# Performance work log

Hardware: AMD Instinct MI355X
Metric: run time of the kernel (lower is better)

Reference implementation:

```python
import jax, jax.numpy as jnp
from jax import lax
import numpy as np

D_MODEL = 128
N_HEADS = 8
N_POINTS = 8
MAX_MAG = 10.0
NEG_SLOPE = 0.1


def conv2d(x, w, b, pad):
    # x: (N, Cin, H, W), w: (Cout, Cin, kh, kw)
    y = lax.conv_general_dilated(x, w, (1, 1), [(pad, pad), (pad, pad)],
                                 dimension_numbers=('NCHW', 'OIHW', 'NCHW'))
    return y + b[None, :, None, None]


def leaky(x):
    return jnp.where(x >= 0, x, NEG_SLOPE * x)


def bilinear_sample(img, grid):
    # img: (B, C, H, W); grid: (B, P, H, W, 2) in [-1, 1] (x, y)
    # Matches torch F.grid_sample(mode='bilinear', padding_mode='zeros', align_corners=False)
    B, C, H, W = img.shape
    x = ((grid[..., 0] + 1.0) * W - 1.0) * 0.5
    y = ((grid[..., 1] + 1.0) * H - 1.0) * 0.5
    x0 = jnp.floor(x)
    y0 = jnp.floor(y)
    wx1 = x - x0
    wy1 = y - y0

    def one(img_b, x0b, y0b, wx1b, wy1b):
        def gather(xi, yi):
            valid = (xi >= 0) & (xi < W) & (yi >= 0) & (yi < H)
            xc = jnp.clip(xi, 0, W - 1).astype(jnp.int32)
            yc = jnp.clip(yi, 0, H - 1).astype(jnp.int32)
            v = img_b[:, yc, xc]  # (C, P, H, W)
            return v * valid
        wx0b = 1.0 - wx1b
        wy0b = 1.0 - wy1b
        v00 = gather(x0b, y0b)
        v01 = gather(x0b + 1, y0b)
        v10 = gather(x0b, y0b + 1)
        v11 = gather(x0b + 1, y0b + 1)
        return (v00 * (wx0b * wy0b) + v01 * (wx1b * wy0b)
                + v10 * (wx0b * wy1b) + v11 * (wx1b * wy1b))

    return jax.vmap(one)(img, x0, y0, wx1, wy1)  # (B, C, P, H, W)


def ss_deform_attn(value, loc):
    # value: (N, nh, d, H, W); loc: (N, nh, P, H, W, 2) in normalized [0,1] coords
    N, nh, d, H, W = value.shape
    P = loc.shape[2]
    v = value.reshape(N * nh, d, H, W)
    grids = (2.0 * loc - 1.0).reshape(N * nh, P, H, W, 2)
    sampled = bilinear_sample(v, grids)  # (N*nh, d, P, H, W)
    # per-location attention logits = <sampled_point, value_at_location>
    scores = jnp.einsum('ndphw,ndhw->nphw', sampled, v)
    aw = jax.nn.softmax(scores, axis=1)
    out = jnp.einsum('ndphw,nphw->ndhw', sampled, aw)
    return out.reshape(N, nh * d, H, W)


def _forward(query, value, reference_points, co_w1, co_b1, co_w2, co_b2,
             co_w3, co_b3, co_w4, co_b4, val_w, val_b, out_w, out_b):
    N, C, H, W = value.shape
    v = conv2d(value, val_w, val_b, 0)
    v = v.reshape(N, N_HEADS, D_MODEL // N_HEADS, H, W)
    o = leaky(conv2d(query, co_w1, co_b1, 1))
    o = leaky(conv2d(o, co_w2, co_b2, 1))
    o = leaky(conv2d(o, co_w3, co_b3, 1))
    o = conv2d(o, co_w4, co_b4, 1)
    o = MAX_MAG * jnp.tanh(o)
    offsets = o.reshape(N, N_HEADS, N_POINTS, H, W, 2)
    norm = jnp.array([W, H], dtype=o.dtype)  # (x, y) normalizer
    loc = reference_points[:, None, None, :, :, :] + offsets / norm
    out = ss_deform_attn(v, loc)
    return conv2d(out, out_w, out_b, 0)


def setup_inputs() -> dict:
    key = jax.random.key(0)
    ks = jax.random.split(key, 12)
    N, H, W = 4, 80, 80

    def w_init(k, shape):
        fan_in = shape[1] * shape[2] * shape[3]
        return jax.random.normal(k, shape, jnp.float32) / np.sqrt(fan_in)

    return {
        'query': jax.random.normal(ks[0], (N, 2 * D_MODEL, H, W), jnp.float32),
        'value': jax.random.normal(ks[1], (N, D_MODEL, H, W), jnp.float32),
        'reference_points': jax.random.uniform(ks[2], (N, H, W, 2), jnp.float32),
        'co_w1': w_init(ks[3], (D_MODEL, 2 * D_MODEL, 3, 3)),
        'co_b1': jnp.zeros((D_MODEL,), jnp.float32),
        'co_w2': w_init(ks[4], (D_MODEL, D_MODEL, 3, 3)),
        'co_b2': jnp.zeros((D_MODEL,), jnp.float32),
        'co_w3': w_init(ks[5], (D_MODEL, D_MODEL, 3, 3)),
        'co_b3': jnp.zeros((D_MODEL,), jnp.float32),
        'co_w4': w_init(ks[6], (N_HEADS * N_POINTS * 2, D_MODEL, 3, 3)),
        'co_b4': jnp.zeros((N_HEADS * N_POINTS * 2,), jnp.float32),
        'val_w': w_init(ks[7], (D_MODEL, D_MODEL, 1, 1)),
        'val_b': jnp.zeros((D_MODEL,), jnp.float32),
        'out_w': w_init(ks[8], (D_MODEL, D_MODEL, 1, 1)),
        'out_b': jnp.zeros((D_MODEL,), jnp.float32),
    }


def reference(query, value, reference_points, co_w1, co_b1, co_w2, co_b2,
              co_w3, co_b3, co_w4, co_b4, val_w, val_b, out_w, out_b):
    return _forward(query, value, reference_points, co_w1, co_b1, co_w2, co_b2,
                    co_w3, co_b3, co_w4, co_b4, val_w, val_b, out_w, out_b)
```

## Files before the change

kernel.cpp:

```cpp
#include <hip/hip_runtime.h>
#include <math.h>

#define Hh 80
#define Ww 80
#define HW 6400
#define PS 6724
#define NB 4

typedef _Float16 half8 __attribute__((ext_vector_type(8)));
typedef _Float16 half4v __attribute__((ext_vector_type(4)));
typedef float f32x16 __attribute__((ext_vector_type(16)));

__device__ __forceinline__ void gload16(const _Float16* g, _Float16* l) {
    __builtin_amdgcn_global_load_lds(
        (const __attribute__((address_space(1))) void*)g,
        (__attribute__((address_space(3))) void*)l, 16, 0, 0);
}

#define WAITVM(N) asm volatile("s_waitcnt vmcnt(" #N ")" ::: "memory")

__device__ __forceinline__ void barrier_mem() {
    asm volatile("" ::: "memory");
    __builtin_amdgcn_s_barrier();
    asm volatile("" ::: "memory");
}

__device__ inline void wblob_one(const float* src, _Float16* dst, int CI, int d) {
    int NC = CI / 32;
    int j = d & 7;
    int l = (d >> 3) & 63;
    int h = (d >> 9) & 1;
    int rest = d >> 10;
    int tap = rest % 9;
    rest /= 9;
    int c = rest % NC;
    int CT = rest / NC;
    int co = CT * 32 + (l & 31);
    int ci = c * 32 + h * 16 + (l >> 5) * 8 + j;
    dst[d] = (_Float16)src[((size_t)co * CI + ci) * 9 + tap];
}

__device__ inline void wblob1x1_one(const float* src, _Float16* dst, int d) {
    int j = d & 7;
    int l = (d >> 3) & 63;
    int c = (d >> 9) & 7;
    int CT = d >> 12;
    int co = CT * 32 + (l & 31);
    int ci = c * 16 + (l >> 5) * 8 + j;
    dst[d] = (_Float16)src[co * 128 + ci];
}

__device__ inline int padsite(int p) {
    if (p < 82) return p;
    if (p < 164) return 81 * 82 + (p - 82);
    if (p < 244) return (p - 163) * 82;
    return (p - 243) * 82 + 81;
}

__global__ __launch_bounds__(256) void prep_all(
    const float* __restrict__ w1, const float* __restrict__ w2,
    const float* __restrict__ w3, const float* __restrict__ w4,
    const float* __restrict__ vw, const float* __restrict__ ow,
    _Float16* __restrict__ b1, _Float16* __restrict__ b2,
    _Float16* __restrict__ b3, _Float16* __restrict__ b4,
    _Float16* __restrict__ bv, _Float16* __restrict__ bo,
    int* __restrict__ qh_i, int* __restrict__ hA_i, int* __restrict__ hB_i,
    const float* __restrict__ query, const float* __restrict__ value,
    _Float16* __restrict__ q_h, _Float16* __restrict__ v_h) {
    __shared__ _Float16 T[64 * 264];
    const int blk = blockIdx.x;
    const int t = threadIdx.x;

    if (blk < 4304) {
        int idx = blk * 256 + t;
        if (idx < 294912) { wblob_one(w1, b1, 256, idx); return; }
        idx -= 294912;
        if (idx < 147456) { wblob_one(w2, b2, 128, idx); return; }
        idx -= 147456;
        if (idx < 147456) { wblob_one(w3, b3, 128, idx); return; }
        idx -= 147456;
        if (idx < 147456) { wblob_one(w4, b4, 128, idx); return; }
        idx -= 147456;
        if (idx < 16384) { wblob1x1_one(vw, bv, idx); return; }
        idx -= 16384;
        if (idx < 16384) { wblob1x1_one(ow, bo, idx); return; }
        idx -= 16384;
        if (idx < 165888) {
            int n = idx / 41472, rr = idx % 41472;
            int c = rr / 5184, r2 = rr % 5184;
            int p = r2 >> 4, k = r2 & 15;
            qh_i[((size_t)(n * 8 + c) * PS + padsite(p)) * 16 + k] = 0;
            return;
        }
        idx -= 165888;
        if (idx < 82944) {
            int n = idx / 20736, rr = idx % 20736;
            int c = rr / 5184, r2 = rr % 5184;
            int p = r2 >> 4, k = r2 & 15;
            hA_i[((size_t)(n * 4 + c) * PS + padsite(p)) * 16 + k] = 0;
            return;
        }
        idx -= 82944;
        if (idx < 82944) {
            int n = idx / 20736, rr = idx % 20736;
            int c = rr / 5184, r2 = rr % 5184;
            int p = r2 >> 4, k = r2 & 15;
            hB_i[((size_t)(n * 4 + c) * PS + padsite(p)) * 16 + k] = 0;
        }
        return;
    }

    if (blk < 4704) {
        const int b = blk - 4304;
        const int xcd = b & 7, n = xcd & 3, hi = xcd >> 2;
        const int s0 = hi * 3200 + (b >> 3) * 64;
        constexpr int CI = 256, ST = CI + 8;
        for (int idx = t; idx < 64 * CI; idx += 256) {
            int ci = idx >> 6, sl = idx & 63;
            T[sl * ST + ci] = (_Float16)query[((size_t)n * CI + ci) * HW + s0 + sl];
        }
        __syncthreads();
        for (int idx = t; idx < 64 * 32; idx += 256) {
            int q = idx & 31, sl = idx >> 5;
            int s = s0 + sl, yy = s / 80, xx = s % 80;
            int c = q >> 2, off = (q & 3) * 8;
            *(int4*)(q_h + ((size_t)(n * 8 + c) * PS + (yy + 1) * 82 + (xx + 1)) * 32 + off) =
                *(const int4*)(&T[sl * ST + q * 8]);
        }
        return;
    }

    {
        const int b = blk - 4704;
        const int xcd = b & 7, n = xcd & 3, hi = xcd >> 2;
        const int s0 = hi * 3200 + (b >> 3) * 64;
        constexpr int CI = 128, ST = CI + 8;
        for (int idx = t; idx < 64 * CI; idx += 256) {
            int ci = idx >> 6, sl = idx & 63;
            T[sl * ST + ci] = (_Float16)value[((size_t)n * CI + ci) * HW + s0 + sl];
        }
        __syncthreads();
        for (int idx = t; idx < 64 * 16; idx += 256) {
            int q = idx & 15, sl = idx >> 4;
            *(int4*)(v_h + ((size_t)n * HW + s0 + sl) * CI + q * 8) =
                *(const int4*)(&T[sl * ST + q * 8]);
        }
    }
}

template <int NCp, int ACT>
__global__ __launch_bounds__(256, 2) void conv3x3_mfma(
    const _Float16* __restrict__ in, const _Float16* __restrict__ wblob,
    const float* __restrict__ bias, void* __restrict__ outp) {
    constexpr int NS = NCp * 18;
    __shared__ _Float16 Abuf[2][24 * 512];
    __shared__ _Float16 Bbuf[2][6 * 1024];

    const int b = blockIdx.x;
    const int xcd = b & 7, n = xcd & 3, hi = xcd >> 2;
    const int r = b >> 3;
    const int x0 = (r % 5) * 16, y0 = hi * 40 + (r / 5) * 4;
    const int t = threadIdx.x;
    const int w = t >> 6, l = t & 63;
    const int lane31 = l & 31, lhalf = l >> 5;
    const int lx = lane31 & 15, lyw = lane31 >> 4;
    const int si = l & 15, g8 = l >> 4;

    const _Float16* bplane0 = in + (size_t)(n * NCp) * PS * 32;
    const _Float16* wA = wblob + (size_t)w * NS * 512 + l * 8;

    f32x16 acc0 = {}, acc1 = {};

    auto stageA = [&](int grp) {
        const _Float16* asrc = wA + (size_t)grp * 6 * 512;
        _Float16* adst = &Abuf[grp & 1][w * 512];
#pragma unroll
        for (int k2 = 0; k2 < 6; ++k2)
            gload16(asrc + (size_t)k2 * 512, adst + (size_t)(k2 * 4) * 512);
    };
    auto stageB = [&](const _Float16* plane, int par) {
#pragma unroll
        for (int j = 0; j < 3; ++j) {
            const int m = 3 * w + j, rr = m >> 1, sg = m & 1;
            gload16(plane + ((size_t)((y0 + rr) * 82 + x0 + sg * 16 + si)) * 32 + g8 * 8,
                    &Bbuf[par][rr * 1024 + sg * 512]);
        }
    };
    auto compute6 = [&](int gi, const _Float16* ab, const _Float16* bb) {
#pragma unroll
        for (int k = 0; k < 6; ++k) {
            const int u = gi * 6 + k;
            const int tap = u >> 1, h = u & 1;
            const int dy = tap / 3, dx = tap % 3;
            half8 a = *(const half8*)&ab[(k * 4 + w) * 512 + l * 8];
            const int cx = lx + dx;
            const int boff = (cx >> 4) * 512 + (h * 2 + lhalf) * 128 + (cx & 15) * 8;
            half8 b0 = *(const half8*)&bb[(lyw + dy) * 1024 + boff];
            half8 b1 = *(const half8*)&bb[(lyw + 2 + dy) * 1024 + boff];
            acc0 = __builtin_amdgcn_mfma_f32_32x32x16_f16(a, b0, acc0, 0, 0, 0);
            acc1 = __builtin_amdgcn_mfma_f32_32x32x16_f16(a, b1, acc1, 0, 0, 0);
        }
    };

    stageA(0);
    stageB(bplane0, 0);

    const _Float16* bplane = bplane0;
#pragma unroll 1
    for (int c = 0; c < NCp - 1; ++c) {
        const _Float16* bplaneN = bplane + (size_t)PS * 32;
        const _Float16* bb = Bbuf[c & 1];
        stageA(3 * c + 1);
        WAITVM(6);
        barrier_mem();
        compute6(0, Abuf[(3 * c) & 1], bb);
        barrier_mem();
        stageA(3 * c + 2);
        WAITVM(6);
        barrier_mem();
        compute6(1, Abuf[(3 * c + 1) & 1], bb);
        barrier_mem();
        stageA(3 * c + 3);
        stageB(bplaneN, (c + 1) & 1);
        WAITVM(9);
        barrier_mem();
        compute6(2, Abuf[(3 * c + 2) & 1], bb);
        barrier_mem();
        bplane = bplaneN;
    }
    {
        const int c = NCp - 1;
        const _Float16* bb = Bbuf[c & 1];
        stageA(3 * c + 1);
        WAITVM(6);
        barrier_mem();
        compute6(0, Abuf[(3 * c) & 1], bb);
        barrier_mem();
        stageA(3 * c + 2);
        WAITVM(6);
        barrier_mem();
        compute6(1, Abuf[(3 * c + 1) & 1], bb);
        barrier_mem();
        WAITVM(0);
        barrier_mem();
        compute6(2, Abuf[(3 * c + 2) & 1], bb);
    }

    const int x = x0 + lx;
#pragma unroll
    for (int f = 0; f < 2; ++f) {
        const f32x16& acc = f ? acc1 : acc0;
        const int y = y0 + lyw + 2 * f;
#pragma unroll
        for (int q = 0; q < 4; ++q) {
            const int inner = 8 * q + 4 * lhalf;
            const int co0 = w * 32 + inner;
            float v[4];
#pragma unroll
            for (int i = 0; i < 4; ++i) {
                float vv = acc[q * 4 + i] + bias[co0 + i];
                if (ACT == 1) vv = (vv >= 0.f) ? vv : 0.1f * vv;
                else vv = 10.f * tanhf(vv);
                v[i] = vv;
            }
            if (ACT == 1) {
                half4v hv = {(_Float16)v[0], (_Float16)v[1], (_Float16)v[2], (_Float16)v[3]};
                *(half4v*)((_Float16*)outp +
                    ((size_t)(n * 4 + w) * PS + (y + 1) * 82 + (x + 1)) * 32 + inner) = hv;
            } else {
                float4 fv = {v[0], v[1], v[2], v[3]};
                *(float4*)((float*)outp + ((size_t)n * HW + y * 80 + x) * 128 + co0) = fv;
            }
        }
    }
}

template <int MODE>
__global__ __launch_bounds__(256) void conv1x1_mfma(
    const _Float16* __restrict__ in, const _Float16* __restrict__ wblob,
    const float* __restrict__ bias, float* __restrict__ outp) {
    const int b = blockIdx.x;
    const int xcd = b & 7, n = xcd & 3, hi = xcd >> 2;
    const int r = b >> 3;
    const int coH = r & 1, strip = r >> 1;
    const int t = threadIdx.x;
    const int w = t >> 6, l = t & 63;
    const int lane31 = l & 31, lhalf = l >> 5;
    const int s = hi * 3200 + strip * 128 + w * 32 + lane31;

    const _Float16* pB = in + (size_t)(n * HW + s) * 128 + lhalf * 8;
    const _Float16* pA0 = wblob + (size_t)(coH * 2) * 8 * 512 + l * 8;
    const _Float16* pA1 = pA0 + 8 * 512;

    half8 bB[8], bA0[8], bA1[8];
#pragma unroll
    for (int c = 0; c < 8; ++c) {
        bB[c]  = *(const half8*)(pB + c * 16);
        bA0[c] = *(const half8*)(pA0 + (size_t)c * 512);
        bA1[c] = *(const half8*)(pA1 + (size_t)c * 512);
    }
    f32x16 acc0 = {}, acc1 = {};
#pragma unroll
    for (int c = 0; c < 8; ++c) {
        acc0 = __builtin_amdgcn_mfma_f32_32x32x16_f16(bA0[c], bB[c], acc0, 0, 0, 0);
        acc1 = __builtin_amdgcn_mfma_f32_32x32x16_f16(bA1[c], bB[c], acc1, 0, 0, 0);
    }

#pragma unroll
    for (int ct = 0; ct < 2; ++ct) {
        const f32x16& acc = ct ? acc1 : acc0;
#pragma unroll
        for (int q = 0; q < 4; ++q) {
            const int co0 = coH * 64 + ct * 32 + 8 * q + 4 * lhalf;
            if (MODE == 0) {
                const int hd = co0 >> 4, dd = co0 & 15;
                float4 fv = {acc[4 * q + 0] + bias[co0 + 0], acc[4 * q + 1] + bias[co0 + 1],
                             acc[4 * q + 2] + bias[co0 + 2], acc[4 * q + 3] + bias[co0 + 3]};
                *(float4*)&outp[((size_t)(n * 8 + hd) * HW + s) * 16 + dd] = fv;
            } else {
#pragma unroll
                for (int i = 0; i < 4; ++i)
                    outp[(size_t)(n * 128 + co0 + i) * HW + s] = acc[4 * q + i] + bias[co0 + i];
            }
        }
    }
}

__global__ __launch_bounds__(256, 2) void deform_attn_kernel(
    const float* __restrict__ v_s, const float* __restrict__ offs,
    const float* __restrict__ ref, _Float16* __restrict__ att) {
    const int slice = blockIdx.x;
    const int n = slice >> 3, hd = slice & 7;
    const int t = threadIdx.x;
    const int s = blockIdx.y * 64 + (t >> 2);
    const int d0 = (t & 3) * 4;
    const int nb = n * 8 + hd;
    const float* vbase = v_s + (size_t)nb * (HW * 16) + d0;

    const float4 cv = *(const float4*)&v_s[((size_t)nb * HW + s) * 16 + d0];
    const float rx = ref[(size_t)(n * HW + s) * 2 + 0] * 80.f - 0.5f;
    const float ry = ref[(size_t)(n * HW + s) * 2 + 1] * 80.f - 0.5f;

    const int e = (s >= 3200) ? 1 : 0;
    const float* ob0 = offs + ((size_t)n * HW + (2 * s - e * HW)) * 128 + hd * 16 + e;

    float4 oxv[4], oyv[4];
#pragma unroll
    for (int i = 0; i < 4; ++i) {
        oxv[i] = *(const float4*)(ob0 + i * 4);
        oyv[i] = *(const float4*)(ob0 + 128 + i * 4);
    }
    float ox[8], oy[8];
#pragma unroll
    for (int i = 0; i < 4; ++i) {
        ox[2 * i] = oxv[i].x; ox[2 * i + 1] = oxv[i].z;
        oy[2 * i] = oyv[i].x; oy[2 * i + 1] = oyv[i].z;
    }

    float wx1[8], wy1[8];
    int ix[8], iy[8];
#pragma unroll
    for (int p = 0; p < 8; ++p) {
        const float px = rx + ox[p];
        const float py = ry + oy[p];
        const float fx = floorf(px), fy = floorf(py);
        ix[p] = (int)fx; iy[p] = (int)fy;
        wx1[p] = px - fx; wy1[p] = py - fy;
    }

    float4 g[8][4];
#pragma unroll
    for (int p = 0; p < 8; ++p) {
        const int xc0 = min(max(ix[p], 0), 79),     xc1 = min(max(ix[p] + 1, 0), 79);
        const int yc0 = min(max(iy[p], 0), 79),     yc1 = min(max(iy[p] + 1, 0), 79);
        const int r0 = yc0 * 80, r1 = yc1 * 80;
        g[p][0] = *(const float4*)(vbase + (size_t)(r0 + xc0) * 16);
        g[p][1] = *(const float4*)(vbase + (size_t)(r0 + xc1) * 16);
        g[p][2] = *(const float4*)(vbase + (size_t)(r1 + xc0) * 16);
        g[p][3] = *(const float4*)(vbase + (size_t)(r1 + xc1) * 16);
    }

    float4 sampled[8];
    float score[8];
#pragma unroll
    for (int p = 0; p < 8; ++p) {
        const float vx0 = (ix[p] >= 0 && ix[p] < Ww) ? 1.f : 0.f;
        const float vx1 = (ix[p] + 1 >= 0 && ix[p] + 1 < Ww) ? 1.f : 0.f;
        const float vy0 = (iy[p] >= 0 && iy[p] < Hh) ? 1.f : 0.f;
        const float vy1 = (iy[p] + 1 >= 0 && iy[p] + 1 < Hh) ? 1.f : 0.f;
        const float wx0 = 1.f - wx1[p], wy0 = 1.f - wy1[p];
        const float w00 = wx0 * wy0 * vx0 * vy0;
        const float w01 = wx1[p] * wy0 * vx1 * vy0;
        const float w10 = wx0 * wy1[p] * vx0 * vy1;
        const float w11 = wx1[p] * wy1[p] * vx1 * vy1;
        float4 sv;
        sv.x = g[p][0].x * w00 + g[p][1].x * w01 + g[p][2].x * w10 + g[p][3].x * w11;
        sv.y = g[p][0].y * w00 + g[p][1].y * w01 + g[p][2].y * w10 + g[p][3].y * w11;
        sv.z = g[p][0].z * w00 + g[p][1].z * w01 + g[p][2].z * w10 + g[p][3].z * w11;
        sv.w = g[p][0].w * w00 + g[p][1].w * w01 + g[p][2].w * w10 + g[p][3].w * w11;
        sampled[p] = sv;
        float sc = sv.x * cv.x + sv.y * cv.y + sv.z * cv.z + sv.w * cv.w;
        sc += __shfl_xor(sc, 1);
        sc += __shfl_xor(sc, 2);
        score[p] = sc;
    }

    float m = score[0];
#pragma unroll
    for (int p = 1; p < 8; ++p) m = fmaxf(m, score[p]);
    float sum = 0.f, aw[8];
#pragma unroll
    for (int p = 0; p < 8; ++p) {
        aw[p] = __expf(score[p] - m);
        sum += aw[p];
    }
    const float inv = 1.f / sum;
    float4 o = {0.f, 0.f, 0.f, 0.f};
#pragma unroll
    for (int p = 0; p < 8; ++p) {
        o.x += aw[p] * sampled[p].x;
        o.y += aw[p] * sampled[p].y;
        o.z += aw[p] * sampled[p].z;
        o.w += aw[p] * sampled[p].w;
    }
    o.x *= inv; o.y *= inv; o.z *= inv; o.w *= inv;

    half4v hv = {(_Float16)o.x, (_Float16)o.y, (_Float16)o.z, (_Float16)o.w};
    *(half4v*)&att[((size_t)n * HW + s) * 128 + hd * 16 + d0] = hv;
}

extern "C" void kernel_launch(void* const* d_in, const int* in_sizes, int n_in,
                              void* d_out, int out_size, void* d_ws, size_t ws_size,
                              hipStream_t stream) {
    const float* query = (const float*)d_in[0];
    const float* value = (const float*)d_in[1];
    const float* ref   = (const float*)d_in[2];
    const float* co_w1 = (const float*)d_in[3];
    const float* co_b1 = (const float*)d_in[4];
    const float* co_w2 = (const float*)d_in[5];
    const float* co_b2 = (const float*)d_in[6];
    const float* co_w3 = (const float*)d_in[7];
    const float* co_b3 = (const float*)d_in[8];
    const float* co_w4 = (const float*)d_in[9];
    const float* co_b4 = (const float*)d_in[10];
    const float* val_w = (const float*)d_in[11];
    const float* val_b = (const float*)d_in[12];
    const float* out_w = (const float*)d_in[13];
    const float* out_b = (const float*)d_in[14];

    char* ws = (char*)d_ws;
    size_t o = 0;
    auto alloc = [&](size_t bytes) { char* p = ws + o; o += (bytes + 255) & ~(size_t)255; return p; };

    _Float16* wb2 = (_Float16*)alloc(147456 * 2);
    _Float16* wb3 = (_Float16*)alloc(147456 * 2);
    _Float16* wb4 = (_Float16*)alloc(147456 * 2);
    _Float16* wbv = (_Float16*)alloc(16384 * 2);
    _Float16* wbo = (_Float16*)alloc(16384 * 2);
    char* vsR = alloc(3276800 * 4);
    float* v_s = (float*)vsR;
    _Float16* wb1 = (_Float16*)vsR;
    _Float16* v_h = (_Float16*)alloc((size_t)NB * HW * 128 * 2);
    char* R1 = alloc((size_t)NB * 8 * PS * 32 * 2);
    _Float16* q_h = (_Float16*)R1;
    float* o4 = (float*)R1;
    char* R2 = alloc((size_t)NB * 4 * PS * 32 * 2 * 2);
    _Float16* hA = (_Float16*)R2;
    _Float16* hB = (_Float16*)(R2 + (size_t)NB * 4 * PS * 32 * 2);
    _Float16* att_h = (_Float16*)R2;

    prep_all<<<5104, 256, 0, stream>>>(co_w1, co_w2, co_w3, co_w4, val_w, out_w,
                                       wb1, wb2, wb3, wb4, wbv, wbo,
                                       (int*)q_h, (int*)hA, (int*)hB,
                                       query, value, q_h, v_h);

    conv3x3_mfma<8, 1><<<400, 256, 0, stream>>>(q_h, wb1, co_b1, hA);

    conv1x1_mfma<0><<<400, 256, 0, stream>>>(v_h, wbv, val_b, v_s);

    conv3x3_mfma<4, 1><<<400, 256, 0, stream>>>(hA, wb2, co_b2, hB);
    conv3x3_mfma<4, 1><<<400, 256, 0, stream>>>(hB, wb3, co_b3, hA);
    conv3x3_mfma<4, 2><<<400, 256, 0, stream>>>(hA, wb4, co_b4, o4);

    deform_attn_kernel<<<dim3(32, 100), 256, 0, stream>>>(v_s, o4, ref, att_h);

    conv1x1_mfma<1><<<400, 256, 0, stream>>>(att_h, wbo, out_b, (float*)d_out);
}
```

Baseline: 229.6 us.

## Load conv weights straight into registers and pipeline channel pairs with fewer barriers

The MFMA conv kernel stops staging the weight (A) fragments through LDS. It now loads them from global memory directly into two alternating register sets, so the next group's weights are fetched while the current group computes. The channel loop is unrolled by pairs and alternates between the two LDS input buffers. That drops the per-group barriers to one wait and barrier per channel and removes the A-side LDS traffic. The cost is more VGPR pressure and weights re-read from cache by every block, and the kernel now requires an even channel-chunk count.

After: 223.1 us. 1.03x faster.

```diff
diff --git a/kernel.cpp b/kernel.cpp
--- a/kernel.cpp
+++ b/kernel.cpp
@@ -18,6 +18,7 @@
 }
 
 #define WAITVM(N) asm volatile("s_waitcnt vmcnt(" #N ")" ::: "memory")
+#define FENCE() asm volatile("" ::: "memory")
 
 __device__ __forceinline__ void barrier_mem() {
     asm volatile("" ::: "memory");
@@ -153,7 +154,7 @@
     const _Float16* __restrict__ in, const _Float16* __restrict__ wblob,
     const float* __restrict__ bias, void* __restrict__ outp) {
     constexpr int NS = NCp * 18;
-    __shared__ _Float16 Abuf[2][24 * 512];
+    static_assert((NCp & 1) == 0, "pair loop needs even NCp");
     __shared__ _Float16 Bbuf[2][6 * 1024];
 
     const int b = blockIdx.x;
@@ -170,14 +171,8 @@
     const _Float16* wA = wblob + (size_t)w * NS * 512 + l * 8;
 
     f32x16 acc0 = {}, acc1 = {};
-
-    auto stageA = [&](int grp) {
-        const _Float16* asrc = wA + (size_t)grp * 6 * 512;
-        _Float16* adst = &Abuf[grp & 1][w * 512];
-#pragma unroll
-        for (int k2 = 0; k2 < 6; ++k2)
-            gload16(asrc + (size_t)k2 * 512, adst + (size_t)(k2 * 4) * 512);
-    };
+    half8 aA[6], aB[6];
+
     auto stageB = [&](const _Float16* plane, int par) {
 #pragma unroll
         for (int j = 0; j < 3; ++j) {
@@ -186,64 +181,67 @@
                     &Bbuf[par][rr * 1024 + sg * 512]);
         }
     };
-    auto compute6 = [&](int gi, const _Float16* ab, const _Float16* bb) {
+    auto loadA6 = [&](half8 (&ar)[6], int grp) {
+        const _Float16* asrc = wA + (size_t)grp * 6 * 512;
+#pragma unroll
+        for (int k2 = 0; k2 < 6; ++k2)
+            ar[k2] = *(const half8*)(asrc + (size_t)k2 * 512);
+    };
+    auto compute6 = [&](int gi, const half8 (&ar)[6], const _Float16* bb) {
 #pragma unroll
         for (int k = 0; k < 6; ++k) {
             const int u = gi * 6 + k;
             const int tap = u >> 1, h = u & 1;
             const int dy = tap / 3, dx = tap % 3;
-            half8 a = *(const half8*)&ab[(k * 4 + w) * 512 + l * 8];
             const int cx = lx + dx;
             const int boff = (cx >> 4) * 512 + (h * 2 + lhalf) * 128 + (cx & 15) * 8;
             half8 b0 = *(const half8*)&bb[(lyw + dy) * 1024 + boff];
             half8 b1 = *(const half8*)&bb[(lyw + 2 + dy) * 1024 + boff];
-            acc0 = __builtin_amdgcn_mfma_f32_32x32x16_f16(a, b0, acc0, 0, 0, 0);
-            acc1 = __builtin_amdgcn_mfma_f32_32x32x16_f16(a, b1, acc1, 0, 0, 0);
+            acc0 = __builtin_amdgcn_mfma_f32_32x32x16_f16(ar[k], b0, acc0, 0, 0, 0);
+            acc1 = __builtin_amdgcn_mfma_f32_32x32x16_f16(ar[k], b1, acc1, 0, 0, 0);
         }
     };
 
-    stageA(0);
     stageB(bplane0, 0);
-
-    const _Float16* bplane = bplane0;
+    loadA6(aA, 0);
+    WAITVM(0);
+    barrier_mem();
+
 #pragma unroll 1
-    for (int c = 0; c < NCp - 1; ++c) {
-        const _Float16* bplaneN = bplane + (size_t)PS * 32;
-        const _Float16* bb = Bbuf[c & 1];
-        stageA(3 * c + 1);
-        WAITVM(6);
+    for (int cp = 0; cp < NCp / 2; ++cp) {
+        const int c0 = 2 * cp;
+        const bool lastp = (cp == NCp / 2 - 1);
+        const _Float16* plane1 = bplane0 + (size_t)(c0 + 1) * PS * 32;
+        const _Float16* plane2 = bplane0 + (size_t)(c0 + 2) * PS * 32;
+        loadA6(aB, c0 * 3 + 1);
+        stageB(plane1, 1);
+        FENCE();
+        compute6(0, aA, Bbuf[0]);
+        loadA6(aA, c0 * 3 + 2);
+        FENCE();
+        compute6(1, aB, Bbuf[0]);
+        loadA6(aB, c0 * 3 + 3);
+        FENCE();
+        compute6(2, aA, Bbuf[0]);
+        WAITVM(12);
         barrier_mem();
-        compute6(0, Abuf[(3 * c) & 1], bb);
-        barrier_mem();
-        stageA(3 * c + 2);
-        WAITVM(6);
-        barrier_mem();
-        compute6(1, Abuf[(3 * c + 1) & 1], bb);
-        barrier_mem();
-        stageA(3 * c + 3);
-        stageB(bplaneN, (c + 1) & 1);
-        WAITVM(9);
-        barrier_mem();
-        compute6(2, Abuf[(3 * c + 2) & 1], bb);
-        barrier_mem();
-        bplane = bplaneN;
-    }
-    {
-        const int c = NCp - 1;
-        const _Float16* bb = Bbuf[c & 1];
-        stageA(3 * c + 1);
-        WAITVM(6);
-        barrier_mem();
-        compute6(0, Abuf[(3 * c) & 1], bb);
-        barrier_mem();
-        stageA(3 * c + 2);
-        WAITVM(6);
-        barrier_mem();
-        compute6(1, Abuf[(3 * c + 1) & 1], bb);
-        barrier_mem();
-        WAITVM(0);
-        barrier_mem();
-        compute6(2, Abuf[(3 * c + 2) & 1], bb);
+        loadA6(aA, c0 * 3 + 4);
+        if (!lastp) stageB(plane2, 0);
+        FENCE();
+        compute6(0, aB, Bbuf[1]);
+        loadA6(aB, c0 * 3 + 5);
+        FENCE();
+        compute6(1, aA, Bbuf[1]);
+        if (!lastp) {
+            loadA6(aA, c0 * 3 + 6);
+            FENCE();
+            compute6(2, aB, Bbuf[1]);
+            WAITVM(12);
+            barrier_mem();
+        } else {
+            FENCE();
+            compute6(2, aB, Bbuf[1]);
+        }
     }
 
     const int x = x0 + lx;
```
